# Optimization experiments

Hardware: AMD Instinct MI355X
Metric: run time of the kernel (lower is better)

The kernel has to match this reference:

```python
import jax, jax.numpy as jnp
import numpy as np

B, L, D, U = 8, 512, 256, 32

def setup_inputs() -> dict:
    key = jax.random.key(0)
    ks = jax.random.split(key, 6)
    g = lambda k, shape: jax.random.normal(k, shape, dtype=jnp.float32) * (2.0 / sum(shape)) ** 0.5
    return {
        "x": jax.random.normal(ks[0], (B, L, D), dtype=jnp.float32),
        "Wt": g(ks[1], (D, U)),
        "Wx": g(ks[2], (D, U)),
        "bh": jnp.zeros((U,), dtype=jnp.float32),
        "Wa": g(ks[3], (U, 1)),
        "ba": jnp.zeros((1,), dtype=jnp.float32),
    }

def reference(x, Wt, Wx, bh, Wa, ba):
    # q: [B,L,1,U], k: [B,1,L,U]
    q = jnp.einsum('bld,du->blu', x, Wt)[:, :, None, :]
    k = jnp.einsum('bld,du->blu', x, Wx)[:, None, :, :]
    beta = jnp.tanh(q + k + bh)                      # [B,L,L,U]
    alpha = jnp.einsum('bstu,u->bst', beta, Wa[:, 0]) + ba[0]  # [B,L,L]
    a = jax.nn.softmax(alpha, axis=-1)               # softmax over keys
    c_r = jnp.einsum('bst,btd->bsd', a, x)           # [B,L,D]
    return c_r
```

## Files before the change

kernel.cpp:

```cpp
#include <hip/hip_runtime.h>

#define B 8
#define L 512
#define D 256
#define U 32
#define ST 8
#define QKR 8

#define K2E    2.885390081777927f
#define KLOG2E 1.4426950408889634f

__global__ __launch_bounds__(256) void qk_kernel(
    const float* __restrict__ x,
    const float* __restrict__ Wt,
    const float* __restrict__ Wx,
    const float* __restrict__ bh,
    float* __restrict__ qb,
    float* __restrict__ kk)
{
    __shared__ float  xs[QKR][D + 1];
    __shared__ float4 pq[3][QKR][8];
    __shared__ float4 pk[3][QKR][8];

    const int b    = blockIdx.x & 7;
    const int tile = blockIdx.x >> 3;
    const int row0 = b * L + tile * QKR;
    const int tid  = threadIdx.x;

    const float4* xg = (const float4*)(x + row0 * D);
    #pragma unroll
    for (int i = tid; i < QKR * D / 4; i += 256) {
        float4 v = xg[i];
        int r = i >> 6;
        int c = (i & 63) << 2;
        xs[r][c] = v.x; xs[r][c + 1] = v.y; xs[r][c + 2] = v.z; xs[r][c + 3] = v.w;
    }
    __syncthreads();

    const int dq = tid >> 6;
    const int r  = (tid >> 3) & 7;
    const int g  = tid & 7;
    const float4* __restrict__ Wt4 = (const float4*)Wt;
    const float4* __restrict__ Wx4 = (const float4*)Wx;

    float4 qa = {0.f, 0.f, 0.f, 0.f};
    float4 ka = {0.f, 0.f, 0.f, 0.f};
    const int d0 = dq * (D / 4);
    #pragma unroll 8
    for (int dd = 0; dd < D / 4; ++dd) {
        const int d = d0 + dd;
        float  xv = xs[r][d];
        float4 wt = Wt4[d * 8 + g];
        float4 wx = Wx4[d * 8 + g];
        qa.x = fmaf(xv, wt.x, qa.x); qa.y = fmaf(xv, wt.y, qa.y);
        qa.z = fmaf(xv, wt.z, qa.z); qa.w = fmaf(xv, wt.w, qa.w);
        ka.x = fmaf(xv, wx.x, ka.x); ka.y = fmaf(xv, wx.y, ka.y);
        ka.z = fmaf(xv, wx.z, ka.z); ka.w = fmaf(xv, wx.w, ka.w);
    }

    if (dq > 0) { pq[dq - 1][r][g] = qa; pk[dq - 1][r][g] = ka; }
    __syncthreads();
    if (dq == 0) {
        #pragma unroll
        for (int w = 0; w < 3; ++w) {
            float4 a = pq[w][r][g], c = pk[w][r][g];
            qa.x += a.x; qa.y += a.y; qa.z += a.z; qa.w += a.w;
            ka.x += c.x; ka.y += c.y; ka.z += c.z; ka.w += c.w;
        }
        float4 b4 = ((const float4*)bh)[g];
        qa.x += b4.x; qa.y += b4.y; qa.z += b4.z; qa.w += b4.w;
        const int row = row0 + r;
        ((float4*)qb)[row * 8 + g] = qa;
        ((float4*)kk)[row * 8 + g] = ka;
    }
}

__device__ __forceinline__ float bcast(float v, int lane) {
    return __int_as_float(__builtin_amdgcn_readlane(__float_as_int(v), lane));
}

__global__ __launch_bounds__(512) void attn_kernel(
    const float* __restrict__ x,
    const float* __restrict__ qb,
    const float* __restrict__ kk,
    const float* __restrict__ Wa,
    const float* __restrict__ ba,
    float* __restrict__ out)
{
    const int blk = blockIdx.x;
    const int b   = blk & 7;
    const int s0  = (blk >> 3) * ST;
    const int tid = threadIdx.x;
    const int wv  = tid >> 6;
    const int ln  = tid & 63;

    __shared__ float4 part[7][ST][64];
    __shared__ float  redm[ST][8];
    __shared__ float  reds[ST][8];

    float kv[U];
    {
        const float4* k4 = (const float4*)(kk + (b * L + tid) * U);
        #pragma unroll
        for (int c = 0; c < 8; ++c) {
            float4 v = k4[c];
            kv[4*c]   = v.x * K2E; kv[4*c+1] = v.y * K2E;
            kv[4*c+2] = v.z * K2E; kv[4*c+3] = v.w * K2E;
        }
    }
    float wa2[U], sWa = 0.f;
    {
        const float4* w4 = (const float4*)Wa;
        #pragma unroll
        for (int c = 0; c < 8; ++c) {
            float4 v = w4[c];
            wa2[4*c]   = v.x * (-2.f * KLOG2E);
            wa2[4*c+1] = v.y * (-2.f * KLOG2E);
            wa2[4*c+2] = v.z * (-2.f * KLOG2E);
            wa2[4*c+3] = v.w * (-2.f * KLOG2E);
            sWa += (v.x + v.y) + (v.z + v.w);
        }
    }
    const float base = (sWa + ba[0]) * KLOG2E;

    const float* __restrict__ qrow = qb + (b * L + s0) * U;
    float avK[ST];
    #pragma unroll 1
    for (int s = 0; s < ST; ++s) {
        const float* __restrict__ q = qrow + s * U;
        float acc = base;
        #pragma unroll
        for (int u = 0; u < U; ++u) {
            float z = fmaf(q[u], K2E, kv[u]);
            float e = __builtin_amdgcn_exp2f(z);
            float r = __builtin_amdgcn_rcpf(e + 1.f);
            acc = fmaf(r, wa2[u], acc);
        }
        avK[s] = acc;
    }

    {
        float mw0,mw1,mw2,mw3,mw4,mw5,mw6,mw7;
        float m[ST];
        #pragma unroll
        for (int s = 0; s < ST; ++s) {
            float v = avK[s];
            #pragma unroll
            for (int off = 1; off < 64; off <<= 1) v = fmaxf(v, __shfl_xor(v, off));
            m[s] = v;
        }
        mw0=m[0];mw1=m[1];mw2=m[2];mw3=m[3];mw4=m[4];mw5=m[5];mw6=m[6];mw7=m[7];
        if (ln == 0) {
            redm[0][wv]=mw0; redm[1][wv]=mw1; redm[2][wv]=mw2; redm[3][wv]=mw3;
            redm[4][wv]=mw4; redm[5][wv]=mw5; redm[6][wv]=mw6; redm[7][wv]=mw7;
        }
    }
    __syncthreads();
    float ew[ST];
    {
        float sm[ST];
        #pragma unroll
        for (int s = 0; s < ST; ++s) {
            float gm = redm[s][0];
            #pragma unroll
            for (int w = 1; w < 8; ++w) gm = fmaxf(gm, redm[s][w]);
            float e = __builtin_amdgcn_exp2f(avK[s] - gm);
            ew[s] = e;
            float ss = e;
            #pragma unroll
            for (int off = 1; off < 64; off <<= 1) ss += __shfl_xor(ss, off);
            sm[s] = ss;
        }
        if (ln == 0) {
            reds[0][wv]=sm[0]; reds[1][wv]=sm[1]; reds[2][wv]=sm[2]; reds[3][wv]=sm[3];
            reds[4][wv]=sm[4]; reds[5][wv]=sm[5]; reds[6][wv]=sm[6]; reds[7][wv]=sm[7];
        }
    }
    __syncthreads();
    float inv[ST];
    #pragma unroll
    for (int s = 0; s < ST; ++s) {
        float ss = reds[s][0];
        #pragma unroll
        for (int w = 1; w < 8; ++w) ss += reds[s][w];
        inv[s] = __builtin_amdgcn_rcpf(ss);
    }

    const float4* __restrict__ x4 = (const float4*)(x + b * L * D);
    const int tbase = wv * 64;

    float4 acc[ST];
    #pragma unroll
    for (int s = 0; s < ST; ++s) acc[s] = make_float4(0.f, 0.f, 0.f, 0.f);

    #pragma unroll 1
    for (int j = 0; j < 64; j += 4) {
        float4 xv[4];
        #pragma unroll
        for (int c = 0; c < 4; ++c)
            xv[c] = x4[(tbase + j + c) * 64 + ln];
        #pragma unroll
        for (int c = 0; c < 4; ++c) {
            #pragma unroll
            for (int s = 0; s < ST; ++s) {
                float a = bcast(ew[s], j + c);
                acc[s].x = fmaf(a, xv[c].x, acc[s].x);
                acc[s].y = fmaf(a, xv[c].y, acc[s].y);
                acc[s].z = fmaf(a, xv[c].z, acc[s].z);
                acc[s].w = fmaf(a, xv[c].w, acc[s].w);
            }
        }
    }

    if (wv > 0) {
        #pragma unroll
        for (int s = 0; s < ST; ++s) part[wv - 1][s][ln] = acc[s];
    }
    __syncthreads();
    if (wv == 0) {
        float4* __restrict__ out4 = (float4*)out;
        #pragma unroll
        for (int s = 0; s < ST; ++s) {
            float4 r = acc[s];
            #pragma unroll
            for (int w = 0; w < 7; ++w) {
                float4 p = part[w][s][ln];
                r.x += p.x; r.y += p.y; r.z += p.z; r.w += p.w;
            }
            const float iv = inv[s];
            r.x *= iv; r.y *= iv; r.z *= iv; r.w *= iv;
            out4[(b * L + s0 + s) * 64 + ln] = r;
        }
    }
}

extern "C" void kernel_launch(void* const* d_in, const int* in_sizes, int n_in,
                              void* d_out, int out_size, void* d_ws, size_t ws_size,
                              hipStream_t stream)
{
    const float* x  = (const float*)d_in[0];
    const float* Wt = (const float*)d_in[1];
    const float* Wx = (const float*)d_in[2];
    const float* bh = (const float*)d_in[3];
    const float* Wa = (const float*)d_in[4];
    const float* ba = (const float*)d_in[5];
    float* out = (float*)d_out;

    float* qb = (float*)d_ws;
    float* kk = qb + B * L * U;

    qk_kernel<<<B * L / QKR, 256, 0, stream>>>(x, Wt, Wx, bh, qb, kk);
    attn_kernel<<<B * (L / ST), 512, 0, stream>>>(x, qb, kk, Wa, ba, out);
}
```

Baseline: 121.5 us.

## Use fp16 MFMA for attention-weighted sum with transposed fp16 x

The qk kernel now also writes a transposed fp16 copy of x. The attention kernel handles 16 query rows per 1024-thread block, stores the softmax numerators as fp16 in shared memory, and computes a·x with 16x16x32 fp16 MFMA instead of scalar FMAs with readlane broadcasts. This removes the scalar weighted-sum loop and its cross-wave partial reduction. In exchange it lowers precision to fp16 inputs, using a +10 exponent shift to keep small weights representable, and adds an extra fp16 write of x.

```diff
diff --git a/kernel.cpp b/kernel.cpp
--- a/kernel.cpp
+++ b/kernel.cpp
@@ -4,11 +4,14 @@
 #define L 512
 #define D 256
 #define U 32
-#define ST 8
+#define ST 16
 #define QKR 8
 
 #define K2E    2.885390081777927f
 #define KLOG2E 1.4426950408889634f
+
+typedef __attribute__((ext_vector_type(8))) _Float16 half8;
+typedef __attribute__((ext_vector_type(4))) float    float4v;
 
 __global__ __launch_bounds__(256) void qk_kernel(
     const float* __restrict__ x,
@@ -16,7 +19,8 @@
     const float* __restrict__ Wx,
     const float* __restrict__ bh,
     float* __restrict__ qb,
-    float* __restrict__ kk)
+    float* __restrict__ kk,
+    _Float16* __restrict__ xT)
 {
     __shared__ float  xs[QKR][D + 1];
     __shared__ float4 pq[3][QKR][8];
@@ -36,6 +40,14 @@
         xs[r][c] = v.x; xs[r][c + 1] = v.y; xs[r][c + 2] = v.z; xs[r][c + 3] = v.w;
     }
     __syncthreads();
+
+    {
+        const int d = tid;
+        half8 h;
+        #pragma unroll
+        for (int r = 0; r < QKR; ++r) h[r] = (_Float16)xs[r][d];
+        *(half8*)(xT + (b * D + d) * L + tile * QKR) = h;
+    }
 
     const int dq = tid >> 6;
     const int r  = (tid >> 3) & 7;
@@ -75,12 +87,8 @@
     }
 }
 
-__device__ __forceinline__ float bcast(float v, int lane) {
-    return __int_as_float(__builtin_amdgcn_readlane(__float_as_int(v), lane));
-}
-
-__global__ __launch_bounds__(512) void attn_kernel(
-    const float* __restrict__ x,
+__global__ __launch_bounds__(1024) void attn_kernel(
+    const _Float16* __restrict__ xT,
     const float* __restrict__ qb,
     const float* __restrict__ kk,
     const float* __restrict__ Wa,
@@ -93,14 +101,18 @@
     const int tid = threadIdx.x;
     const int wv  = tid >> 6;
     const int ln  = tid & 63;
-
-    __shared__ float4 part[7][ST][64];
-    __shared__ float  redm[ST][8];
-    __shared__ float  reds[ST][8];
+    const int t   = tid & 511;
+    const int sh  = tid >> 9;
+    const int wl  = wv & 7;
+
+    __shared__ _Float16 a_sh[ST][L + 8];
+    __shared__ float redm[ST][8];
+    __shared__ float reds[ST][8];
+    __shared__ float inv_sh[ST];
 
     float kv[U];
     {
-        const float4* k4 = (const float4*)(kk + (b * L + tid) * U);
+        const float4* k4 = (const float4*)(kk + (b * L + t) * U);
         #pragma unroll
         for (int c = 0; c < 8; ++c) {
             float4 v = k4[c];
@@ -108,129 +120,78 @@
             kv[4*c+2] = v.z * K2E; kv[4*c+3] = v.w * K2E;
         }
     }
-    float wa2[U], sWa = 0.f;
-    {
-        const float4* w4 = (const float4*)Wa;
-        #pragma unroll
-        for (int c = 0; c < 8; ++c) {
-            float4 v = w4[c];
-            wa2[4*c]   = v.x * (-2.f * KLOG2E);
-            wa2[4*c+1] = v.y * (-2.f * KLOG2E);
-            wa2[4*c+2] = v.z * (-2.f * KLOG2E);
-            wa2[4*c+3] = v.w * (-2.f * KLOG2E);
-            sWa += (v.x + v.y) + (v.z + v.w);
-        }
-    }
+    float sWa = 0.f;
+    #pragma unroll
+    for (int u = 0; u < U; ++u) sWa += Wa[u];
     const float base = (sWa + ba[0]) * KLOG2E;
 
-    const float* __restrict__ qrow = qb + (b * L + s0) * U;
-    float avK[ST];
+    const float* __restrict__ qrow = qb + (b * L + s0 + sh * 8) * U;
+    float avK[8];
     #pragma unroll 1
-    for (int s = 0; s < ST; ++s) {
+    for (int s = 0; s < 8; ++s) {
         const float* __restrict__ q = qrow + s * U;
-        float acc = base;
+        float tacc = 0.f;
         #pragma unroll
         for (int u = 0; u < U; ++u) {
             float z = fmaf(q[u], K2E, kv[u]);
             float e = __builtin_amdgcn_exp2f(z);
             float r = __builtin_amdgcn_rcpf(e + 1.f);
-            acc = fmaf(r, wa2[u], acc);
+            tacc = fmaf(r, Wa[u], tacc);
         }
-        avK[s] = acc;
-    }
-
-    {
-        float mw0,mw1,mw2,mw3,mw4,mw5,mw6,mw7;
-        float m[ST];
-        #pragma unroll
-        for (int s = 0; s < ST; ++s) {
-            float v = avK[s];
-            #pragma unroll
-            for (int off = 1; off < 64; off <<= 1) v = fmaxf(v, __shfl_xor(v, off));
-            m[s] = v;
-        }
-        mw0=m[0];mw1=m[1];mw2=m[2];mw3=m[3];mw4=m[4];mw5=m[5];mw6=m[6];mw7=m[7];
-        if (ln == 0) {
-            redm[0][wv]=mw0; redm[1][wv]=mw1; redm[2][wv]=mw2; redm[3][wv]=mw3;
-            redm[4][wv]=mw4; redm[5][wv]=mw5; redm[6][wv]=mw6; redm[7][wv]=mw7;
-        }
-    }
-    __syncthreads();
-    float ew[ST];
-    {
-        float sm[ST];
-        #pragma unroll
-        for (int s = 0; s < ST; ++s) {
-            float gm = redm[s][0];
-            #pragma unroll
-            for (int w = 1; w < 8; ++w) gm = fmaxf(gm, redm[s][w]);
-            float e = __builtin_amdgcn_exp2f(avK[s] - gm);
-            ew[s] = e;
-            float ss = e;
-            #pragma unroll
-            for (int off = 1; off < 64; off <<= 1) ss += __shfl_xor(ss, off);
-            sm[s] = ss;
-        }
-        if (ln == 0) {
-            reds[0][wv]=sm[0]; reds[1][wv]=sm[1]; reds[2][wv]=sm[2]; reds[3][wv]=sm[3];
-            reds[4][wv]=sm[4]; reds[5][wv]=sm[5]; reds[6][wv]=sm[6]; reds[7][wv]=sm[7];
-        }
-    }
-    __syncthreads();
-    float inv[ST];
-    #pragma unroll
-    for (int s = 0; s < ST; ++s) {
-        float ss = reds[s][0];
-        #pragma unroll
-        for (int w = 1; w < 8; ++w) ss += reds[s][w];
-        inv[s] = __builtin_amdgcn_rcpf(ss);
-    }
-
-    const float4* __restrict__ x4 = (const float4*)(x + b * L * D);
-    const int tbase = wv * 64;
-
-    float4 acc[ST];
-    #pragma unroll
-    for (int s = 0; s < ST; ++s) acc[s] = make_float4(0.f, 0.f, 0.f, 0.f);
-
-    #pragma unroll 1
-    for (int j = 0; j < 64; j += 4) {
-        float4 xv[4];
-        #pragma unroll
-        for (int c = 0; c < 4; ++c)
-            xv[c] = x4[(tbase + j + c) * 64 + ln];
-        #pragma unroll
-        for (int c = 0; c < 4; ++c) {
-            #pragma unroll
-            for (int s = 0; s < ST; ++s) {
-                float a = bcast(ew[s], j + c);
-                acc[s].x = fmaf(a, xv[c].x, acc[s].x);
-                acc[s].y = fmaf(a, xv[c].y, acc[s].y);
-                acc[s].z = fmaf(a, xv[c].z, acc[s].z);
-                acc[s].w = fmaf(a, xv[c].w, acc[s].w);
-            }
-        }
-    }
-
-    if (wv > 0) {
-        #pragma unroll
-        for (int s = 0; s < ST; ++s) part[wv - 1][s][ln] = acc[s];
-    }
-    __syncthreads();
-    if (wv == 0) {
-        float4* __restrict__ out4 = (float4*)out;
-        #pragma unroll
-        for (int s = 0; s < ST; ++s) {
-            float4 r = acc[s];
-            #pragma unroll
-            for (int w = 0; w < 7; ++w) {
-                float4 p = part[w][s][ln];
-                r.x += p.x; r.y += p.y; r.z += p.z; r.w += p.w;
-            }
-            const float iv = inv[s];
-            r.x *= iv; r.y *= iv; r.z *= iv; r.w *= iv;
-            out4[(b * L + s0 + s) * 64 + ln] = r;
-        }
+        avK[s] = fmaf(tacc, -2.f * KLOG2E, base);
+    }
+
+    #pragma unroll
+    for (int s = 0; s < 8; ++s) {
+        float v = avK[s];
+        #pragma unroll
+        for (int off = 1; off < 64; off <<= 1) v = fmaxf(v, __shfl_xor(v, off));
+        if (ln == 0) redm[sh * 8 + s][wl] = v;
+    }
+    __syncthreads();
+    float e2[8];
+    #pragma unroll
+    for (int s = 0; s < 8; ++s) {
+        float gm = redm[sh * 8 + s][0];
+        #pragma unroll
+        for (int w = 1; w < 8; ++w) gm = fmaxf(gm, redm[sh * 8 + s][w]);
+        float e = __builtin_amdgcn_exp2f(avK[s] - gm + 10.f);
+        e2[s] = e;
+        float ss = e;
+        #pragma unroll
+        for (int off = 1; off < 64; off <<= 1) ss += __shfl_xor(ss, off);
+        if (ln == 0) reds[sh * 8 + s][wl] = ss;
+    }
+    __syncthreads();
+    if (tid < ST) {
+        float ss = 0.f;
+        #pragma unroll
+        for (int w = 0; w < 8; ++w) ss += reds[tid][w];
+        inv_sh[tid] = __builtin_amdgcn_rcpf(ss);
+    }
+    #pragma unroll
+    for (int s = 0; s < 8; ++s)
+        a_sh[sh * 8 + s][t] = (_Float16)e2[s];
+    __syncthreads();
+
+    const int n0   = wv * 16;
+    const int row  = ln & 15;
+    const int quad = ln >> 4;
+    const _Float16* __restrict__ xrow = xT + (b * D + n0 + row) * L + quad * 8;
+    const _Float16* __restrict__ arow = &a_sh[row][quad * 8];
+
+    float4v acc = {0.f, 0.f, 0.f, 0.f};
+    #pragma unroll 4
+    for (int kc = 0; kc < 16; ++kc) {
+        half8 af = *(const half8*)(arow + kc * 32);
+        half8 bf = *(const half8*)(xrow + kc * 32);
+        acc = __builtin_amdgcn_mfma_f32_16x16x32_f16(af, bf, acc, 0, 0, 0);
+    }
+
+    #pragma unroll
+    for (int r = 0; r < 4; ++r) {
+        const int m = quad * 4 + r;
+        out[(b * L + s0 + m) * D + n0 + row] = acc[r] * inv_sh[m];
     }
 }
 
@@ -246,9 +207,10 @@
     const float* ba = (const float*)d_in[5];
     float* out = (float*)d_out;
 
-    float* qb = (float*)d_ws;
-    float* kk = qb + B * L * U;
-
-    qk_kernel<<<B * L / QKR, 256, 0, stream>>>(x, Wt, Wx, bh, qb, kk);
-    attn_kernel<<<B * (L / ST), 512, 0, stream>>>(x, qb, kk, Wa, ba, out);
+    float*    qb = (float*)d_ws;
+    float*    kk = qb + B * L * U;
+    _Float16* xT = (_Float16*)(kk + B * L * U);
+
+    qk_kernel<<<B * L / QKR, 256, 0, stream>>>(x, Wt, Wx, bh, qb, kk, xT);
+    attn_kernel<<<B * (L / ST), 1024, 0, stream>>>(xT, qb, kk, Wa, ba, out);
 }
```

Result: faster. 117.8 us (-3.1%).
